# Optimization experiments

Measured on AMD Instinct MI355X. Metric: run time of the kernel, lower is better.

The kernel has to match this reference:

```python
import jax, jax.numpy as jnp
import numpy as np

B, I, H, T = 65536, 64, 64, 16  # batch, input_size, hidden_size, type_num


def setup_inputs() -> dict:
    key = jax.random.key(0)
    ks = jax.random.split(key, 10)
    s = 0.1  # ~1/sqrt(H) init scale like torch GRUCell
    return {
        "x": jax.random.normal(ks[0], (B, I), jnp.float32),
        "typ": jax.random.randint(ks[1], (B,), 0, T, jnp.int32),
        "c": jax.random.normal(ks[2], (B, H), jnp.float32),
        "registers": jax.random.normal(ks[3], (B, T, H), jnp.float32),
        # per-type GRUCell bank (stacked across types)
        "Wih": jax.random.normal(ks[4], (T, 3 * H, I), jnp.float32) * s,
        "Whh": jax.random.normal(ks[5], (T, 3 * H, H), jnp.float32) * s,
        "bih": jax.random.normal(ks[6], (T, 3 * H), jnp.float32) * s,
        "bhh": jax.random.normal(ks[7], (T, 3 * H), jnp.float32) * s,
        # core GRUCell: input = flattened registers (T*H)
        "cWih": jax.random.normal(ks[8], (3 * H, T * H), jnp.float32) * s,
        "cWhh": jax.random.normal(ks[9], (3 * H, H), jnp.float32) * s,
        "cbih": jnp.zeros((3 * H,), jnp.float32),
        "cbhh": jnp.zeros((3 * H,), jnp.float32),
    }


def _gru(gi, gh, h):
    # torch.nn.GRUCell math; gi/gh: (..., 3H), h: (..., H)
    ir, iz, in_ = jnp.split(gi, 3, axis=-1)
    hr, hz, hn = jnp.split(gh, 3, axis=-1)
    r = jax.nn.sigmoid(ir + hr)
    z = jax.nn.sigmoid(iz + hz)
    n = jnp.tanh(in_ + r * hn)
    return (1.0 - z) * n + z * h


def reference(x, typ, c, registers, Wih, Whh, bih, bhh, cWih, cWhh, cbih, cbhh):
    # Bank of T GRUCells, all run on the same input x with per-type hidden = registers[:, t]
    gi = jnp.einsum('bi,tgi->btg', x, Wih) + bih[None]            # (B,T,3H)
    gh = jnp.einsum('bth,tgh->btg', registers, Whh) + bhh[None]   # (B,T,3H)
    hidden_tmp = _gru(gi, gh, registers)                          # (B,T,H)

    # Gather/scatter register update: only slot typ[b] takes its GRU output,
    # all other slots keep the old register (exactly what hidden_all[N, I] does).
    mask = (jnp.arange(T)[None, :] == typ[:, None])[..., None]    # (B,T,1)
    reg_new = jnp.where(mask, hidden_tmp, registers)              # (B,T,H)

    # core_v2: core GRUCell over flattened registers with state c
    xflat = reg_new.reshape(B, T * H)
    cgi = xflat @ cWih.T + cbih
    cgh = c @ cWhh.T + cbhh
    core = _gru(cgi, cgh, c)                                      # (B,H)
    return core
```

## Files before the change

### kernel.cpp

```cpp
#include <hip/hip_runtime.h>
#include <hip/hip_bf16.h>

typedef unsigned short u16;
typedef unsigned int u32;
typedef __bf16 bf16x8 __attribute__((ext_vector_type(8)));
typedef float f32x4 __attribute__((ext_vector_type(4)));


__device__ __forceinline__ u16 f2bf(float f) {
  union { float f; u32 u; } v; v.f = f;
  u32 u = v.u;
  return (u16)((u + 0x7fffu + ((u >> 16) & 1u)) >> 16);
}
__device__ __forceinline__ float bf2f(u16 h) {
  union { u32 u; float f; } v; v.u = ((u32)h) << 16;
  return v.f;
}
__device__ __forceinline__ u32 pk2(float a, float b) {
  union { __hip_bfloat162 h; u32 u; } v;
  v.h = __float22bfloat162_rn(float2{a, b});
  return v.u;
}
__device__ __forceinline__ bf16x8 pack8(float4 a, float4 b) {
  union { u32 u[4]; bf16x8 v; } r;
  r.u[0] = pk2(a.x, a.y); r.u[1] = pk2(a.z, a.w);
  r.u[2] = pk2(b.x, b.y); r.u[3] = pk2(b.z, b.w);
  return r.v;
}
__device__ __forceinline__ float sigf(float x) { return 1.0f / (1.0f + __expf(-x)); }
__device__ __forceinline__ float tanh_fast(float x) { return 2.0f * sigf(2.0f * x) - 1.0f; }

__device__ __forceinline__ void gl_lds16(const void* g, void* l) {
  __builtin_amdgcn_global_load_lds(
      (const __attribute__((address_space(1))) unsigned int*)g,
      (__attribute__((address_space(3))) unsigned int*)l, 16, 0, 0);
}

__global__ __launch_bounds__(256) void k0_convert(
    const float* __restrict__ Wih, const float* __restrict__ Whh,
    const float* __restrict__ cWih, const float* __restrict__ cWhh,
    u16* __restrict__ wih_bf, u16* __restrict__ whh_bf,
    u16* __restrict__ cwih_bf, u16* __restrict__ cwhh_bf, int* __restrict__ gcnt)
{
  int i = blockIdx.x * 256 + threadIdx.x;
  if (blockIdx.x == 0 && threadIdx.x < 16) gcnt[threadIdx.x] = 0;
  if (i < 196608) {
    wih_bf[i]  = f2bf(Wih[i]);
    whh_bf[i]  = f2bf(Whh[i]);
    cwih_bf[i] = f2bf(cWih[i]);
  }
  if (i < 12288) cwhh_bf[i] = f2bf(cWhh[i]);
}

__global__ __launch_bounds__(256) void k_compact(
    const int* __restrict__ typ, int* __restrict__ gcnt, int* __restrict__ lists)
{
  __shared__ int cnt[16], base[16];
  const int tid = threadIdx.x;
  if (tid < 16) cnt[tid] = 0;
  __syncthreads();
  int r = blockIdx.x * 256 + tid;
  int t = typ[r];
  int rank = atomicAdd(&cnt[t], 1);
  __syncthreads();
  if (tid < 16) base[tid] = atomicAdd(&gcnt[tid], cnt[tid]);
  __syncthreads();
  lists[(size_t)t * 65536 + base[t] + rank] = r;
}

__global__ __launch_bounds__(256, 2) void k1_corr(
    const float* __restrict__ x, const float* __restrict__ regs,
    const u16* __restrict__ wih_bf, const u16* __restrict__ whh_bf,
    const float* __restrict__ bih, const float* __restrict__ bhh,
    const u16* __restrict__ cwih_bf,
    const int* __restrict__ gcnt, const int* __restrict__ lists,
    u16* __restrict__ corr)
{
  const int t = blockIdx.y;
  const int cnt = gcnt[t];
  const int ntiles = (cnt + 15) >> 4;

  const int tid = threadIdx.x;
  const int lane = tid & 63;
  const int w = tid >> 6;
  const int col = lane & 15;
  const int quad = lane >> 4;
  const int hidx = w * 16 + col;
  const f32x4 zero = {0.f, 0.f, 0.f, 0.f};

  bf16x8 bw[3][2], bh[3][2], bc[3][2];
  float vbi[3], vbh[3];
#pragma unroll
  for (int g = 0; g < 3; ++g) {
    const u16* pw = wih_bf + ((size_t)t * 192 + g * 64 + hidx) * 64;
    const u16* ph = whh_bf + ((size_t)t * 192 + g * 64 + hidx) * 64;
    const u16* pc = cwih_bf + (size_t)(g * 64 + hidx) * 1024 + t * 64;
#pragma unroll
    for (int ks = 0; ks < 2; ++ks) {
      bw[g][ks] = *(const bf16x8*)(pw + ks * 32 + quad * 8);
      bh[g][ks] = *(const bf16x8*)(ph + ks * 32 + quad * 8);
      bc[g][ks] = *(const bf16x8*)(pc + ks * 32 + quad * 8);
    }
    vbi[g] = bih[t * 192 + g * 64 + hidx];
    vbh[g] = bhh[t * 192 + g * 64 + hidx];
  }

  __shared__ int s_rows[16];
  __shared__ __align__(16) u16 sD[16 * 72];

  for (int tile = blockIdx.x; tile < ntiles; tile += 32) {
    __syncthreads();
    if (tid < 16) {
      int idx = tile * 16 + tid;
      s_rows[tid] = lists[(size_t)t * 65536 + (idx < cnt ? idx : cnt - 1)];
    }
    __syncthreads();

    const int ra = s_rows[col];
    f32x4 agi[3], agh[3];
#pragma unroll
    for (int g = 0; g < 3; ++g) { agi[g] = zero; agh[g] = zero; }
#pragma unroll
    for (int ks = 0; ks < 2; ++ks) {
      const float* xr = x + (size_t)ra * 64 + ks * 32 + quad * 8;
      const float* hr = regs + (size_t)ra * 1024 + t * 64 + ks * 32 + quad * 8;
      bf16x8 ax = pack8(*(const float4*)xr, *(const float4*)(xr + 4));
      bf16x8 ah = pack8(*(const float4*)hr, *(const float4*)(hr + 4));
#pragma unroll
      for (int g = 0; g < 3; ++g) {
        agi[g] = __builtin_amdgcn_mfma_f32_16x16x32_bf16(ax, bw[g][ks], agi[g], 0, 0, 0);
        agh[g] = __builtin_amdgcn_mfma_f32_16x16x32_bf16(ah, bh[g][ks], agh[g], 0, 0, 0);
      }
    }
#pragma unroll
    for (int rr = 0; rr < 4; ++rr) {
      int m = quad * 4 + rr;
      if (tile * 16 + m < cnt) {
        int r2 = s_rows[m];
        float ir  = agi[0][rr] + vbi[0];
        float iz  = agi[1][rr] + vbi[1];
        float in_ = agi[2][rr] + vbi[2];
        float hr  = agh[0][rr] + vbh[0];
        float hz  = agh[1][rr] + vbh[1];
        float hn  = agh[2][rr] + vbh[2];
        float rg = sigf(ir + hr);
        float zg = sigf(iz + hz);
        float ng = tanh_fast(in_ + rg * hn);
        float hold = regs[(size_t)r2 * 1024 + t * 64 + hidx];
        float hnew = (1.f - zg) * ng + zg * hold;
        sD[m * 72 + hidx] = f2bf(hnew - hold);
      }
    }
    __syncthreads();

    f32x4 acr[3];
#pragma unroll
    for (int g = 0; g < 3; ++g) acr[g] = zero;
#pragma unroll
    for (int ks = 0; ks < 2; ++ks) {
      bf16x8 ad = *(const bf16x8*)(&sD[col * 72 + ks * 32 + quad * 8]);
#pragma unroll
      for (int g = 0; g < 3; ++g)
        acr[g] = __builtin_amdgcn_mfma_f32_16x16x32_bf16(ad, bc[g][ks], acr[g], 0, 0, 0);
    }
#pragma unroll
    for (int rr = 0; rr < 4; ++rr) {
      int m = quad * 4 + rr;
      if (tile * 16 + m < cnt) {
        int r2 = s_rows[m];
#pragma unroll
        for (int g = 0; g < 3; ++g)
          corr[(size_t)r2 * 192 + g * 64 + hidx] = f2bf(acr[g][rr]);
      }
    }
  }
}

__global__ __launch_bounds__(256, 2) void k2_core(
    const float* __restrict__ regs, const float* __restrict__ c,
    const u16* __restrict__ cwih_bf, const u16* __restrict__ cwhh_bf,
    const float* __restrict__ cbih, const float* __restrict__ cbhh,
    const u16* __restrict__ corr, float* __restrict__ out)
{
  __shared__ __align__(16) float sA[2][4096];
  __shared__ __align__(16) u16  sB[2][12288];

  const int tid = threadIdx.x;
  const int b0 = blockIdx.x * 64;
  const int lane = tid & 63;
  const int wv = tid >> 6;
  const int col = lane & 15;
  const int quad = lane >> 4;
  const int hidx = wv * 16 + col;
  const f32x4 zero = {0.f, 0.f, 0.f, 0.f};

  {
#pragma unroll
    for (int s = 0; s < 4; ++s) {
      int i = s * 4 + wv;
      int r = i * 4 + (lane >> 4);
      int grp = lane & 15;
      gl_lds16(regs + (size_t)(b0 + r) * 1024 + ((grp ^ (r & 15)) << 2), &sA[0][i * 256]);
    }
#pragma unroll
    for (int s = 0; s < 6; ++s) {
      int j = s * 4 + wv;
      int n = j * 8 + (lane >> 3);
      int grp = lane & 7;
      gl_lds16(cwih_bf + (size_t)n * 1024 + ((grp ^ (n & 7)) << 3), &sB[0][j * 512]);
    }
  }

  f32x4 agh[4][3];
#pragma unroll
  for (int mt = 0; mt < 4; ++mt)
#pragma unroll
    for (int g = 0; g < 3; ++g) agh[mt][g] = zero;
#pragma unroll
  for (int ks = 0; ks < 2; ++ks) {
    bf16x8 bh2[3];
#pragma unroll
    for (int g = 0; g < 3; ++g)
      bh2[g] = *(const bf16x8*)(cwhh_bf + (size_t)(g * 64 + hidx) * 64 + ks * 32 + quad * 8);
#pragma unroll
    for (int mt = 0; mt < 4; ++mt) {
      const float* cr = c + (size_t)(b0 + mt * 16 + col) * 64 + ks * 32 + quad * 8;
      bf16x8 af = pack8(*(const float4*)cr, *(const float4*)(cr + 4));
#pragma unroll
      for (int g = 0; g < 3; ++g)
        agh[mt][g] = __builtin_amdgcn_mfma_f32_16x16x32_bf16(af, bh2[g], agh[mt][g], 0, 0, 0);
    }
  }

  f32x4 agi[4][3];
#pragma unroll
  for (int mt = 0; mt < 4; ++mt)
#pragma unroll
    for (int g = 0; g < 3; ++g) agi[mt][g] = zero;

  for (int kc = 0; kc < 16; ++kc) {
    __syncthreads();
    if (kc < 15) {
      float* sAn = sA[(kc + 1) & 1];
      u16*   sBn = sB[(kc + 1) & 1];
#pragma unroll
      for (int s = 0; s < 4; ++s) {
        int i = s * 4 + wv;
        int r = i * 4 + (lane >> 4);
        int grp = lane & 15;
        gl_lds16(regs + (size_t)(b0 + r) * 1024 + (kc + 1) * 64 + ((grp ^ (r & 15)) << 2),
                 sAn + i * 256);
      }
#pragma unroll
      for (int s = 0; s < 6; ++s) {
        int j = s * 4 + wv;
        int n = j * 8 + (lane >> 3);
        int grp = lane & 7;
        gl_lds16(cwih_bf + (size_t)n * 1024 + (kc + 1) * 64 + ((grp ^ (n & 7)) << 3),
                 sBn + j * 512);
      }
    }
    const float* sAc = sA[kc & 1];
    const u16*   sBc = sB[kc & 1];
#pragma unroll
    for (int ks = 0; ks < 2; ++ks) {
      bf16x8 bfr[3];
#pragma unroll
      for (int g = 0; g < 3; ++g) {
        int n = g * 64 + hidx;
        int grp = ks * 4 + quad;
        bfr[g] = *(const bf16x8*)(sBc + n * 64 + ((grp ^ (n & 7)) << 3));
      }
#pragma unroll
      for (int mt = 0; mt < 4; ++mt) {
        int r = mt * 16 + col;
        int g0 = ks * 8 + quad * 2;
        float4 q0 = *(const float4*)(sAc + r * 64 + (((g0    ) ^ (r & 15)) << 2));
        float4 q1 = *(const float4*)(sAc + r * 64 + (((g0 + 1) ^ (r & 15)) << 2));
        bf16x8 af = pack8(q0, q1);
#pragma unroll
        for (int g = 0; g < 3; ++g)
          agi[mt][g] = __builtin_amdgcn_mfma_f32_16x16x32_bf16(af, bfr[g], agi[mt][g], 0, 0, 0);
      }
    }
  }

  float e0 = cbih[hidx], e1 = cbih[64 + hidx], e2 = cbih[128 + hidx];
  float d0 = cbhh[hidx], d1 = cbhh[64 + hidx], d2 = cbhh[128 + hidx];
#pragma unroll
  for (int mt = 0; mt < 4; ++mt) {
#pragma unroll
    for (int rr = 0; rr < 4; ++rr) {
      int row = mt * 16 + quad * 4 + rr;
      size_t b = (size_t)(b0 + row);
      float ir  = agi[mt][0][rr] + e0 + bf2f(corr[b * 192 + hidx]);
      float iz  = agi[mt][1][rr] + e1 + bf2f(corr[b * 192 + 64 + hidx]);
      float in_ = agi[mt][2][rr] + e2 + bf2f(corr[b * 192 + 128 + hidx]);
      float hr  = agh[mt][0][rr] + d0;
      float hz  = agh[mt][1][rr] + d1;
      float hn  = agh[mt][2][rr] + d2;
      float rg = sigf(ir + hr);
      float zg = sigf(iz + hz);
      float ng = tanh_fast(in_ + rg * hn);
      float cold = c[b * 64 + hidx];
      out[b * 64 + hidx] = (1.f - zg) * ng + zg * cold;
    }
  }
}

extern "C" void kernel_launch(void* const* d_in, const int* in_sizes, int n_in,
                              void* d_out, int out_size, void* d_ws, size_t ws_size,
                              hipStream_t stream) {
  const float* x    = (const float*)d_in[0];
  const int*   typ  = (const int*)d_in[1];
  const float* c    = (const float*)d_in[2];
  const float* regs = (const float*)d_in[3];
  const float* Wih  = (const float*)d_in[4];
  const float* Whh  = (const float*)d_in[5];
  const float* bih  = (const float*)d_in[6];
  const float* bhh  = (const float*)d_in[7];
  const float* cWih = (const float*)d_in[8];
  const float* cWhh = (const float*)d_in[9];
  const float* cbih = (const float*)d_in[10];
  const float* cbhh = (const float*)d_in[11];
  float* out = (float*)d_out;

  char* ws = (char*)d_ws;
  u16* wih_bf  = (u16*)(ws + 0);
  u16* whh_bf  = (u16*)(ws + 393216);
  u16* cwih_bf = (u16*)(ws + 786432);
  u16* cwhh_bf = (u16*)(ws + 1179648);
  int* gcnt    = (int*)(ws + 1204224);
  int* lists   = (int*)(ws + 1204288);
  u16* corr    = (u16*)(ws + 5398592);

  k0_convert<<<768, 256, 0, stream>>>(Wih, Whh, cWih, cWhh,
                                      wih_bf, whh_bf, cwih_bf, cwhh_bf, gcnt);
  k_compact<<<256, 256, 0, stream>>>(typ, gcnt, lists);
  k1_corr<<<dim3(32, 16), 256, 0, stream>>>(x, regs, wih_bf, whh_bf, bih, bhh,
                                            cwih_bf, gcnt, lists, corr);
  k2_core<<<1024, 256, 0, stream>>>(regs, c, cwih_bf, cwhh_bf, cbih, cbhh, corr, out);
}
```

Baseline: 476.0 us.

## Fuse per-type GRU correction and core GRU into one type-grouped kernel

Merges the per-type correction kernel and the core GRU kernel into a single kernel that processes 64-row tiles of same-type rows. The per-type delta is kept in LDS and fed directly into the core input accumulator, so the bf16 corr buffer no longer round-trips through global memory and one launch disappears. Register rows are now gathered through the row list instead of read contiguously. The cWih tiles are read straight from global (L2) rather than staged in LDS. Each of the 72x16 blocks loops over several tiles with no cross-type load balancing, so uneven type counts can leave some blocks with more work.

```diff
diff --git a/kernel.cpp b/kernel.cpp
--- a/kernel.cpp
+++ b/kernel.cpp
@@ -11,10 +11,6 @@
   union { float f; u32 u; } v; v.f = f;
   u32 u = v.u;
   return (u16)((u + 0x7fffu + ((u >> 16) & 1u)) >> 16);
-}
-__device__ __forceinline__ float bf2f(u16 h) {
-  union { u32 u; float f; } v; v.u = ((u32)h) << 16;
-  return v.f;
 }
 __device__ __forceinline__ u32 pk2(float a, float b) {
   union { __hip_bfloat162 h; u32 u; } v;
@@ -68,125 +64,25 @@
   lists[(size_t)t * 65536 + base[t] + rank] = r;
 }
 
-__global__ __launch_bounds__(256, 2) void k1_corr(
+__global__ __launch_bounds__(256, 2) void k_fused(
     const float* __restrict__ x, const float* __restrict__ regs,
+    const float* __restrict__ c,
     const u16* __restrict__ wih_bf, const u16* __restrict__ whh_bf,
     const float* __restrict__ bih, const float* __restrict__ bhh,
-    const u16* __restrict__ cwih_bf,
+    const u16* __restrict__ cwih_bf, const u16* __restrict__ cwhh_bf,
+    const float* __restrict__ cbih, const float* __restrict__ cbhh,
     const int* __restrict__ gcnt, const int* __restrict__ lists,
-    u16* __restrict__ corr)
+    float* __restrict__ out)
 {
   const int t = blockIdx.y;
   const int cnt = gcnt[t];
-  const int ntiles = (cnt + 15) >> 4;
+  if ((int)blockIdx.x * 64 >= cnt) return;
+
+  __shared__ __align__(16) float sA[2][4096];
+  __shared__ __align__(16) u16  sD[4096];
+  __shared__ int s_rows[64];
 
   const int tid = threadIdx.x;
-  const int lane = tid & 63;
-  const int w = tid >> 6;
-  const int col = lane & 15;
-  const int quad = lane >> 4;
-  const int hidx = w * 16 + col;
-  const f32x4 zero = {0.f, 0.f, 0.f, 0.f};
-
-  bf16x8 bw[3][2], bh[3][2], bc[3][2];
-  float vbi[3], vbh[3];
-#pragma unroll
-  for (int g = 0; g < 3; ++g) {
-    const u16* pw = wih_bf + ((size_t)t * 192 + g * 64 + hidx) * 64;
-    const u16* ph = whh_bf + ((size_t)t * 192 + g * 64 + hidx) * 64;
-    const u16* pc = cwih_bf + (size_t)(g * 64 + hidx) * 1024 + t * 64;
-#pragma unroll
-    for (int ks = 0; ks < 2; ++ks) {
-      bw[g][ks] = *(const bf16x8*)(pw + ks * 32 + quad * 8);
-      bh[g][ks] = *(const bf16x8*)(ph + ks * 32 + quad * 8);
-      bc[g][ks] = *(const bf16x8*)(pc + ks * 32 + quad * 8);
-    }
-    vbi[g] = bih[t * 192 + g * 64 + hidx];
-    vbh[g] = bhh[t * 192 + g * 64 + hidx];
-  }
-
-  __shared__ int s_rows[16];
-  __shared__ __align__(16) u16 sD[16 * 72];
-
-  for (int tile = blockIdx.x; tile < ntiles; tile += 32) {
-    __syncthreads();
-    if (tid < 16) {
-      int idx = tile * 16 + tid;
-      s_rows[tid] = lists[(size_t)t * 65536 + (idx < cnt ? idx : cnt - 1)];
-    }
-    __syncthreads();
-
-    const int ra = s_rows[col];
-    f32x4 agi[3], agh[3];
-#pragma unroll
-    for (int g = 0; g < 3; ++g) { agi[g] = zero; agh[g] = zero; }
-#pragma unroll
-    for (int ks = 0; ks < 2; ++ks) {
-      const float* xr = x + (size_t)ra * 64 + ks * 32 + quad * 8;
-      const float* hr = regs + (size_t)ra * 1024 + t * 64 + ks * 32 + quad * 8;
-      bf16x8 ax = pack8(*(const float4*)xr, *(const float4*)(xr + 4));
-      bf16x8 ah = pack8(*(const float4*)hr, *(const float4*)(hr + 4));
-#pragma unroll
-      for (int g = 0; g < 3; ++g) {
-        agi[g] = __builtin_amdgcn_mfma_f32_16x16x32_bf16(ax, bw[g][ks], agi[g], 0, 0, 0);
-        agh[g] = __builtin_amdgcn_mfma_f32_16x16x32_bf16(ah, bh[g][ks], agh[g], 0, 0, 0);
-      }
-    }
-#pragma unroll
-    for (int rr = 0; rr < 4; ++rr) {
-      int m = quad * 4 + rr;
-      if (tile * 16 + m < cnt) {
-        int r2 = s_rows[m];
-        float ir  = agi[0][rr] + vbi[0];
-        float iz  = agi[1][rr] + vbi[1];
-        float in_ = agi[2][rr] + vbi[2];
-        float hr  = agh[0][rr] + vbh[0];
-        float hz  = agh[1][rr] + vbh[1];
-        float hn  = agh[2][rr] + vbh[2];
-        float rg = sigf(ir + hr);
-        float zg = sigf(iz + hz);
-        float ng = tanh_fast(in_ + rg * hn);
-        float hold = regs[(size_t)r2 * 1024 + t * 64 + hidx];
-        float hnew = (1.f - zg) * ng + zg * hold;
-        sD[m * 72 + hidx] = f2bf(hnew - hold);
-      }
-    }
-    __syncthreads();
-
-    f32x4 acr[3];
-#pragma unroll
-    for (int g = 0; g < 3; ++g) acr[g] = zero;
-#pragma unroll
-    for (int ks = 0; ks < 2; ++ks) {
-      bf16x8 ad = *(const bf16x8*)(&sD[col * 72 + ks * 32 + quad * 8]);
-#pragma unroll
-      for (int g = 0; g < 3; ++g)
-        acr[g] = __builtin_amdgcn_mfma_f32_16x16x32_bf16(ad, bc[g][ks], acr[g], 0, 0, 0);
-    }
-#pragma unroll
-    for (int rr = 0; rr < 4; ++rr) {
-      int m = quad * 4 + rr;
-      if (tile * 16 + m < cnt) {
-        int r2 = s_rows[m];
-#pragma unroll
-        for (int g = 0; g < 3; ++g)
-          corr[(size_t)r2 * 192 + g * 64 + hidx] = f2bf(acr[g][rr]);
-      }
-    }
-  }
-}
-
-__global__ __launch_bounds__(256, 2) void k2_core(
-    const float* __restrict__ regs, const float* __restrict__ c,
-    const u16* __restrict__ cwih_bf, const u16* __restrict__ cwhh_bf,
-    const float* __restrict__ cbih, const float* __restrict__ cbhh,
-    const u16* __restrict__ corr, float* __restrict__ out)
-{
-  __shared__ __align__(16) float sA[2][4096];
-  __shared__ __align__(16) u16  sB[2][12288];
-
-  const int tid = threadIdx.x;
-  const int b0 = blockIdx.x * 64;
   const int lane = tid & 63;
   const int wv = tid >> 6;
   const int col = lane & 15;
@@ -194,116 +90,170 @@
   const int hidx = wv * 16 + col;
   const f32x4 zero = {0.f, 0.f, 0.f, 0.f};
 
-  {
-#pragma unroll
-    for (int s = 0; s < 4; ++s) {
-      int i = s * 4 + wv;
-      int r = i * 4 + (lane >> 4);
-      int grp = lane & 15;
-      gl_lds16(regs + (size_t)(b0 + r) * 1024 + ((grp ^ (r & 15)) << 2), &sA[0][i * 256]);
-    }
-#pragma unroll
-    for (int s = 0; s < 6; ++s) {
-      int j = s * 4 + wv;
-      int n = j * 8 + (lane >> 3);
-      int grp = lane & 7;
-      gl_lds16(cwih_bf + (size_t)n * 1024 + ((grp ^ (n & 7)) << 3), &sB[0][j * 512]);
-    }
+  bf16x8 bw[3][2], bh[3][2], bc[3][2];
+  float vbi[3], vbh[3];
+#pragma unroll
+  for (int g = 0; g < 3; ++g) {
+    const u16* pw = wih_bf + ((size_t)t * 192 + g * 64 + hidx) * 64;
+    const u16* ph = whh_bf + ((size_t)t * 192 + g * 64 + hidx) * 64;
+    const u16* pc = cwih_bf + (size_t)(g * 64 + hidx) * 1024 + t * 64;
+#pragma unroll
+    for (int ks = 0; ks < 2; ++ks) {
+      bw[g][ks] = *(const bf16x8*)(pw + ks * 32 + quad * 8);
+      bh[g][ks] = *(const bf16x8*)(ph + ks * 32 + quad * 8);
+      bc[g][ks] = *(const bf16x8*)(pc + ks * 32 + quad * 8);
+    }
+    vbi[g] = bih[t * 192 + g * 64 + hidx];
+    vbh[g] = bhh[t * 192 + g * 64 + hidx];
   }
-
-  f32x4 agh[4][3];
-#pragma unroll
-  for (int mt = 0; mt < 4; ++mt)
-#pragma unroll
-    for (int g = 0; g < 3; ++g) agh[mt][g] = zero;
-#pragma unroll
-  for (int ks = 0; ks < 2; ++ks) {
-    bf16x8 bh2[3];
-#pragma unroll
-    for (int g = 0; g < 3; ++g)
-      bh2[g] = *(const bf16x8*)(cwhh_bf + (size_t)(g * 64 + hidx) * 64 + ks * 32 + quad * 8);
-#pragma unroll
+  const float e0 = cbih[hidx], e1 = cbih[64 + hidx], e2 = cbih[128 + hidx];
+  const float d0 = cbhh[hidx], d1 = cbhh[64 + hidx], d2 = cbhh[128 + hidx];
+
+  for (int tile = blockIdx.x; tile * 64 < cnt; tile += (int)gridDim.x) {
+    __syncthreads();
+    if (tid < 64) {
+      int idx = tile * 64 + tid;
+      s_rows[tid] = lists[(size_t)t * 65536 + (idx < cnt ? idx : cnt - 1)];
+    }
+    __syncthreads();
+
+    const int grp = lane & 15;
+    const int rsw = wv * 4 + quad;
+    const float* pA[4];
+#pragma unroll
+    for (int s = 0; s < 4; ++s)
+      pA[s] = regs + (size_t)s_rows[s * 16 + wv * 4 + quad] * 1024 + ((grp ^ rsw) << 2);
+
+#pragma unroll
+    for (int s = 0; s < 4; ++s)
+      gl_lds16(pA[s], &sA[0][(s * 4 + wv) * 256]);
+
+#pragma unroll 2
     for (int mt = 0; mt < 4; ++mt) {
-      const float* cr = c + (size_t)(b0 + mt * 16 + col) * 64 + ks * 32 + quad * 8;
-      bf16x8 af = pack8(*(const float4*)cr, *(const float4*)(cr + 4));
+      const int ra = s_rows[mt * 16 + col];
+      f32x4 agi1[3], agh1[3];
+#pragma unroll
+      for (int g = 0; g < 3; ++g) { agi1[g] = zero; agh1[g] = zero; }
+#pragma unroll
+      for (int ks = 0; ks < 2; ++ks) {
+        const float* xr = x + (size_t)ra * 64 + ks * 32 + quad * 8;
+        const float* hr = regs + (size_t)ra * 1024 + t * 64 + ks * 32 + quad * 8;
+        bf16x8 ax = pack8(*(const float4*)xr, *(const float4*)(xr + 4));
+        bf16x8 ah = pack8(*(const float4*)hr, *(const float4*)(hr + 4));
+#pragma unroll
+        for (int g = 0; g < 3; ++g) {
+          agi1[g] = __builtin_amdgcn_mfma_f32_16x16x32_bf16(ax, bw[g][ks], agi1[g], 0, 0, 0);
+          agh1[g] = __builtin_amdgcn_mfma_f32_16x16x32_bf16(ah, bh[g][ks], agh1[g], 0, 0, 0);
+        }
+      }
+#pragma unroll
+      for (int rr = 0; rr < 4; ++rr) {
+        const int m = mt * 16 + quad * 4 + rr;
+        const int r2 = s_rows[m];
+        float ir  = agi1[0][rr] + vbi[0];
+        float iz  = agi1[1][rr] + vbi[1];
+        float in_ = agi1[2][rr] + vbi[2];
+        float hr2 = agh1[0][rr] + vbh[0];
+        float hz  = agh1[1][rr] + vbh[1];
+        float hn  = agh1[2][rr] + vbh[2];
+        float rg = sigf(ir + hr2);
+        float zg = sigf(iz + hz);
+        float ng = tanh_fast(in_ + rg * hn);
+        float hold = regs[(size_t)r2 * 1024 + t * 64 + hidx];
+        float hnew = (1.f - zg) * ng + zg * hold;
+        sD[m * 64 + (((hidx >> 3) ^ (m & 7)) << 3) + (hidx & 7)] = f2bf(hnew - hold);
+      }
+    }
+
+    f32x4 agh[4][3];
+#pragma unroll
+    for (int mt = 0; mt < 4; ++mt)
+#pragma unroll
+      for (int g = 0; g < 3; ++g) agh[mt][g] = zero;
+#pragma unroll
+    for (int ks = 0; ks < 2; ++ks) {
+      bf16x8 bh2[3];
 #pragma unroll
       for (int g = 0; g < 3; ++g)
-        agh[mt][g] = __builtin_amdgcn_mfma_f32_16x16x32_bf16(af, bh2[g], agh[mt][g], 0, 0, 0);
-    }
-  }
-
-  f32x4 agi[4][3];
-#pragma unroll
-  for (int mt = 0; mt < 4; ++mt)
-#pragma unroll
-    for (int g = 0; g < 3; ++g) agi[mt][g] = zero;
-
-  for (int kc = 0; kc < 16; ++kc) {
+        bh2[g] = *(const bf16x8*)(cwhh_bf + (size_t)(g * 64 + hidx) * 64 + ks * 32 + quad * 8);
+#pragma unroll
+      for (int mt = 0; mt < 4; ++mt) {
+        const float* cr = c + (size_t)s_rows[mt * 16 + col] * 64 + ks * 32 + quad * 8;
+        bf16x8 af = pack8(*(const float4*)cr, *(const float4*)(cr + 4));
+#pragma unroll
+        for (int g = 0; g < 3; ++g)
+          agh[mt][g] = __builtin_amdgcn_mfma_f32_16x16x32_bf16(af, bh2[g], agh[mt][g], 0, 0, 0);
+      }
+    }
+
     __syncthreads();
-    if (kc < 15) {
-      float* sAn = sA[(kc + 1) & 1];
-      u16*   sBn = sB[(kc + 1) & 1];
-#pragma unroll
-      for (int s = 0; s < 4; ++s) {
-        int i = s * 4 + wv;
-        int r = i * 4 + (lane >> 4);
-        int grp = lane & 15;
-        gl_lds16(regs + (size_t)(b0 + r) * 1024 + (kc + 1) * 64 + ((grp ^ (r & 15)) << 2),
-                 sAn + i * 256);
-      }
-#pragma unroll
-      for (int s = 0; s < 6; ++s) {
-        int j = s * 4 + wv;
-        int n = j * 8 + (lane >> 3);
-        int grp = lane & 7;
-        gl_lds16(cwih_bf + (size_t)n * 1024 + (kc + 1) * 64 + ((grp ^ (n & 7)) << 3),
-                 sBn + j * 512);
-      }
-    }
-    const float* sAc = sA[kc & 1];
-    const u16*   sBc = sB[kc & 1];
+
+    f32x4 agi[4][3];
+#pragma unroll
+    for (int mt = 0; mt < 4; ++mt)
+#pragma unroll
+      for (int g = 0; g < 3; ++g) agi[mt][g] = zero;
 #pragma unroll
     for (int ks = 0; ks < 2; ++ks) {
-      bf16x8 bfr[3];
-#pragma unroll
-      for (int g = 0; g < 3; ++g) {
-        int n = g * 64 + hidx;
-        int grp = ks * 4 + quad;
-        bfr[g] = *(const bf16x8*)(sBc + n * 64 + ((grp ^ (n & 7)) << 3));
-      }
 #pragma unroll
       for (int mt = 0; mt < 4; ++mt) {
-        int r = mt * 16 + col;
-        int g0 = ks * 8 + quad * 2;
-        float4 q0 = *(const float4*)(sAc + r * 64 + (((g0    ) ^ (r & 15)) << 2));
-        float4 q1 = *(const float4*)(sAc + r * 64 + (((g0 + 1) ^ (r & 15)) << 2));
-        bf16x8 af = pack8(q0, q1);
+        const int m = mt * 16 + col;
+        bf16x8 ad = *(const bf16x8*)(&sD[m * 64 + (((ks * 4 + quad) ^ (m & 7)) << 3)]);
 #pragma unroll
         for (int g = 0; g < 3; ++g)
-          agi[mt][g] = __builtin_amdgcn_mfma_f32_16x16x32_bf16(af, bfr[g], agi[mt][g], 0, 0, 0);
-      }
-    }
-  }
-
-  float e0 = cbih[hidx], e1 = cbih[64 + hidx], e2 = cbih[128 + hidx];
-  float d0 = cbhh[hidx], d1 = cbhh[64 + hidx], d2 = cbhh[128 + hidx];
-#pragma unroll
-  for (int mt = 0; mt < 4; ++mt) {
-#pragma unroll
-    for (int rr = 0; rr < 4; ++rr) {
-      int row = mt * 16 + quad * 4 + rr;
-      size_t b = (size_t)(b0 + row);
-      float ir  = agi[mt][0][rr] + e0 + bf2f(corr[b * 192 + hidx]);
-      float iz  = agi[mt][1][rr] + e1 + bf2f(corr[b * 192 + 64 + hidx]);
-      float in_ = agi[mt][2][rr] + e2 + bf2f(corr[b * 192 + 128 + hidx]);
-      float hr  = agh[mt][0][rr] + d0;
-      float hz  = agh[mt][1][rr] + d1;
-      float hn  = agh[mt][2][rr] + d2;
-      float rg = sigf(ir + hr);
-      float zg = sigf(iz + hz);
-      float ng = tanh_fast(in_ + rg * hn);
-      float cold = c[b * 64 + hidx];
-      out[b * 64 + hidx] = (1.f - zg) * ng + zg * cold;
+          agi[mt][g] = __builtin_amdgcn_mfma_f32_16x16x32_bf16(ad, bc[g][ks], agi[mt][g], 0, 0, 0);
+      }
+    }
+
+    for (int kc = 0; kc < 16; ++kc) {
+      __syncthreads();
+      if (kc < 15) {
+        float* sAn = sA[(kc + 1) & 1];
+#pragma unroll
+        for (int s = 0; s < 4; ++s)
+          gl_lds16(pA[s] + (kc + 1) * 64, sAn + (s * 4 + wv) * 256);
+      }
+      const float* sAc = sA[kc & 1];
+#pragma unroll
+      for (int ks = 0; ks < 2; ++ks) {
+        bf16x8 bfr[3];
+#pragma unroll
+        for (int g = 0; g < 3; ++g)
+          bfr[g] = *(const bf16x8*)(cwih_bf + (size_t)(g * 64 + hidx) * 1024 + kc * 64 + ks * 32 + quad * 8);
+#pragma unroll
+        for (int mt = 0; mt < 4; ++mt) {
+          const int r = mt * 16 + col;
+          const int g0 = ks * 8 + quad * 2;
+          float4 q0 = *(const float4*)(sAc + r * 64 + (((g0    ) ^ (r & 15)) << 2));
+          float4 q1 = *(const float4*)(sAc + r * 64 + (((g0 + 1) ^ (r & 15)) << 2));
+          bf16x8 af = pack8(q0, q1);
+#pragma unroll
+          for (int g = 0; g < 3; ++g)
+            agi[mt][g] = __builtin_amdgcn_mfma_f32_16x16x32_bf16(af, bfr[g], agi[mt][g], 0, 0, 0);
+        }
+      }
+    }
+
+#pragma unroll
+    for (int mt = 0; mt < 4; ++mt) {
+#pragma unroll
+      for (int rr = 0; rr < 4; ++rr) {
+        const int m = mt * 16 + quad * 4 + rr;
+        if (tile * 64 + m < cnt) {
+          const size_t b = (size_t)s_rows[m];
+          float ir  = agi[mt][0][rr] + e0;
+          float iz  = agi[mt][1][rr] + e1;
+          float in_ = agi[mt][2][rr] + e2;
+          float hr2 = agh[mt][0][rr] + d0;
+          float hz  = agh[mt][1][rr] + d1;
+          float hn  = agh[mt][2][rr] + d2;
+          float rg = sigf(ir + hr2);
+          float zg = sigf(iz + hz);
+          float ng = tanh_fast(in_ + rg * hn);
+          float cold = c[b * 64 + hidx];
+          out[b * 64 + hidx] = (1.f - zg) * ng + zg * cold;
+        }
+      }
     }
   }
 }
@@ -332,12 +282,10 @@
   u16* cwhh_bf = (u16*)(ws + 1179648);
   int* gcnt    = (int*)(ws + 1204224);
   int* lists   = (int*)(ws + 1204288);
-  u16* corr    = (u16*)(ws + 5398592);
 
   k0_convert<<<768, 256, 0, stream>>>(Wih, Whh, cWih, cWhh,
                                       wih_bf, whh_bf, cwih_bf, cwhh_bf, gcnt);
   k_compact<<<256, 256, 0, stream>>>(typ, gcnt, lists);
-  k1_corr<<<dim3(32, 16), 256, 0, stream>>>(x, regs, wih_bf, whh_bf, bih, bhh,
-                                            cwih_bf, gcnt, lists, corr);
-  k2_core<<<1024, 256, 0, stream>>>(regs, c, cwih_bf, cwhh_bf, cbih, cbhh, corr, out);
-}
+  k_fused<<<dim3(72, 16), 256, 0, stream>>>(x, regs, c, wih_bf, whh_bf, bih, bhh,
+                                            cwih_bf, cwhh_bf, cbih, cbhh, gcnt, lists, out);
+}
```

Result: slower. 564.3 us (+18.6%).

## Substitute updated register slot directly in core GEMM load instead of correction term

Applied to the files above, without the earlier changes.

Instead of computing a per-row correction (hnew-hold) projected through cWih in k1 and adding it in k2, k1 now writes the fp32 new hidden state for the selected slot, and k2 picks, per row and K-chunk, whether to load from registers or from that slot buffer. This removes the correction MFMA, its LDS staging and sync, and the bf16 corr write and read. It also avoids bf16 rounding of the difference term. In exchange, k2 takes per-lane address selection and reads typ.

```diff
diff --git a/kernel.cpp b/kernel.cpp
--- a/kernel.cpp
+++ b/kernel.cpp
@@ -11,10 +11,6 @@
   union { float f; u32 u; } v; v.f = f;
   u32 u = v.u;
   return (u16)((u + 0x7fffu + ((u >> 16) & 1u)) >> 16);
-}
-__device__ __forceinline__ float bf2f(u16 h) {
-  union { u32 u; float f; } v; v.u = ((u32)h) << 16;
-  return v.f;
 }
 __device__ __forceinline__ u32 pk2(float a, float b) {
   union { __hip_bfloat162 h; u32 u; } v;
@@ -68,13 +64,12 @@
   lists[(size_t)t * 65536 + base[t] + rank] = r;
 }
 
-__global__ __launch_bounds__(256, 2) void k1_corr(
+__global__ __launch_bounds__(256, 2) void k1_gru(
     const float* __restrict__ x, const float* __restrict__ regs,
     const u16* __restrict__ wih_bf, const u16* __restrict__ whh_bf,
     const float* __restrict__ bih, const float* __restrict__ bhh,
-    const u16* __restrict__ cwih_bf,
     const int* __restrict__ gcnt, const int* __restrict__ lists,
-    u16* __restrict__ corr)
+    float* __restrict__ modslot)
 {
   const int t = blockIdx.y;
   const int cnt = gcnt[t];
@@ -88,25 +83,22 @@
   const int hidx = w * 16 + col;
   const f32x4 zero = {0.f, 0.f, 0.f, 0.f};
 
-  bf16x8 bw[3][2], bh[3][2], bc[3][2];
+  bf16x8 bw[3][2], bh[3][2];
   float vbi[3], vbh[3];
 #pragma unroll
   for (int g = 0; g < 3; ++g) {
     const u16* pw = wih_bf + ((size_t)t * 192 + g * 64 + hidx) * 64;
     const u16* ph = whh_bf + ((size_t)t * 192 + g * 64 + hidx) * 64;
-    const u16* pc = cwih_bf + (size_t)(g * 64 + hidx) * 1024 + t * 64;
 #pragma unroll
     for (int ks = 0; ks < 2; ++ks) {
       bw[g][ks] = *(const bf16x8*)(pw + ks * 32 + quad * 8);
       bh[g][ks] = *(const bf16x8*)(ph + ks * 32 + quad * 8);
-      bc[g][ks] = *(const bf16x8*)(pc + ks * 32 + quad * 8);
     }
     vbi[g] = bih[t * 192 + g * 64 + hidx];
     vbh[g] = bhh[t * 192 + g * 64 + hidx];
   }
 
   __shared__ int s_rows[16];
-  __shared__ __align__(16) u16 sD[16 * 72];
 
   for (int tile = blockIdx.x; tile < ntiles; tile += 32) {
     __syncthreads();
@@ -148,29 +140,7 @@
         float ng = tanh_fast(in_ + rg * hn);
         float hold = regs[(size_t)r2 * 1024 + t * 64 + hidx];
         float hnew = (1.f - zg) * ng + zg * hold;
-        sD[m * 72 + hidx] = f2bf(hnew - hold);
-      }
-    }
-    __syncthreads();
-
-    f32x4 acr[3];
-#pragma unroll
-    for (int g = 0; g < 3; ++g) acr[g] = zero;
-#pragma unroll
-    for (int ks = 0; ks < 2; ++ks) {
-      bf16x8 ad = *(const bf16x8*)(&sD[col * 72 + ks * 32 + quad * 8]);
-#pragma unroll
-      for (int g = 0; g < 3; ++g)
-        acr[g] = __builtin_amdgcn_mfma_f32_16x16x32_bf16(ad, bc[g][ks], acr[g], 0, 0, 0);
-    }
-#pragma unroll
-    for (int rr = 0; rr < 4; ++rr) {
-      int m = quad * 4 + rr;
-      if (tile * 16 + m < cnt) {
-        int r2 = s_rows[m];
-#pragma unroll
-        for (int g = 0; g < 3; ++g)
-          corr[(size_t)r2 * 192 + g * 64 + hidx] = f2bf(acr[g][rr]);
+        modslot[(size_t)r2 * 64 + hidx] = hnew;
       }
     }
   }
@@ -178,9 +148,10 @@
 
 __global__ __launch_bounds__(256, 2) void k2_core(
     const float* __restrict__ regs, const float* __restrict__ c,
+    const int* __restrict__ typ, const float* __restrict__ modslot,
     const u16* __restrict__ cwih_bf, const u16* __restrict__ cwhh_bf,
     const float* __restrict__ cbih, const float* __restrict__ cbhh,
-    const u16* __restrict__ corr, float* __restrict__ out)
+    float* __restrict__ out)
 {
   __shared__ __align__(16) float sA[2][4096];
   __shared__ __align__(16) u16  sB[2][12288];
@@ -194,20 +165,32 @@
   const int hidx = wv * 16 + col;
   const f32x4 zero = {0.f, 0.f, 0.f, 0.f};
 
+  const int grp = lane & 15;
+  const float* pA[4];
+  const float* pM[4];
+  int t4[4];
+#pragma unroll
+  for (int s = 0; s < 4; ++s) {
+    int i = s * 4 + wv;
+    int r = i * 4 + (lane >> 4);
+    int swz = (grp ^ (r & 15)) << 2;
+    pA[s] = regs + (size_t)(b0 + r) * 1024 + swz;
+    pM[s] = modslot + (size_t)(b0 + r) * 64 + swz;
+    t4[s] = typ[b0 + r];
+  }
+
   {
 #pragma unroll
     for (int s = 0; s < 4; ++s) {
-      int i = s * 4 + wv;
-      int r = i * 4 + (lane >> 4);
-      int grp = lane & 15;
-      gl_lds16(regs + (size_t)(b0 + r) * 1024 + ((grp ^ (r & 15)) << 2), &sA[0][i * 256]);
+      const float* src = (t4[s] == 0) ? pM[s] : pA[s];
+      gl_lds16(src, &sA[0][(s * 4 + wv) * 256]);
     }
 #pragma unroll
     for (int s = 0; s < 6; ++s) {
       int j = s * 4 + wv;
       int n = j * 8 + (lane >> 3);
-      int grp = lane & 7;
-      gl_lds16(cwih_bf + (size_t)n * 1024 + ((grp ^ (n & 7)) << 3), &sB[0][j * 512]);
+      int grpb = lane & 7;
+      gl_lds16(cwih_bf + (size_t)n * 1024 + ((grpb ^ (n & 7)) << 3), &sB[0][j * 512]);
     }
   }
 
@@ -245,18 +228,15 @@
       u16*   sBn = sB[(kc + 1) & 1];
 #pragma unroll
       for (int s = 0; s < 4; ++s) {
-        int i = s * 4 + wv;
-        int r = i * 4 + (lane >> 4);
-        int grp = lane & 15;
-        gl_lds16(regs + (size_t)(b0 + r) * 1024 + (kc + 1) * 64 + ((grp ^ (r & 15)) << 2),
-                 sAn + i * 256);
+        const float* src = (t4[s] == kc + 1) ? pM[s] : (pA[s] + (kc + 1) * 64);
+        gl_lds16(src, sAn + (s * 4 + wv) * 256);
       }
 #pragma unroll
       for (int s = 0; s < 6; ++s) {
         int j = s * 4 + wv;
         int n = j * 8 + (lane >> 3);
-        int grp = lane & 7;
-        gl_lds16(cwih_bf + (size_t)n * 1024 + (kc + 1) * 64 + ((grp ^ (n & 7)) << 3),
+        int grpb = lane & 7;
+        gl_lds16(cwih_bf + (size_t)n * 1024 + (kc + 1) * 64 + ((grpb ^ (n & 7)) << 3),
                  sBn + j * 512);
       }
     }
@@ -268,8 +248,8 @@
 #pragma unroll
       for (int g = 0; g < 3; ++g) {
         int n = g * 64 + hidx;
-        int grp = ks * 4 + quad;
-        bfr[g] = *(const bf16x8*)(sBc + n * 64 + ((grp ^ (n & 7)) << 3));
+        int grpb = ks * 4 + quad;
+        bfr[g] = *(const bf16x8*)(sBc + n * 64 + ((grpb ^ (n & 7)) << 3));
       }
 #pragma unroll
       for (int mt = 0; mt < 4; ++mt) {
@@ -293,9 +273,9 @@
     for (int rr = 0; rr < 4; ++rr) {
       int row = mt * 16 + quad * 4 + rr;
       size_t b = (size_t)(b0 + row);
-      float ir  = agi[mt][0][rr] + e0 + bf2f(corr[b * 192 + hidx]);
-      float iz  = agi[mt][1][rr] + e1 + bf2f(corr[b * 192 + 64 + hidx]);
-      float in_ = agi[mt][2][rr] + e2 + bf2f(corr[b * 192 + 128 + hidx]);
+      float ir  = agi[mt][0][rr] + e0;
+      float iz  = agi[mt][1][rr] + e1;
+      float in_ = agi[mt][2][rr] + e2;
       float hr  = agh[mt][0][rr] + d0;
       float hz  = agh[mt][1][rr] + d1;
       float hn  = agh[mt][2][rr] + d2;
@@ -332,12 +312,13 @@
   u16* cwhh_bf = (u16*)(ws + 1179648);
   int* gcnt    = (int*)(ws + 1204224);
   int* lists   = (int*)(ws + 1204288);
-  u16* corr    = (u16*)(ws + 5398592);
+  float* modslot = (float*)(ws + 5398592);
 
   k0_convert<<<768, 256, 0, stream>>>(Wih, Whh, cWih, cWhh,
                                       wih_bf, whh_bf, cwih_bf, cwhh_bf, gcnt);
   k_compact<<<256, 256, 0, stream>>>(typ, gcnt, lists);
-  k1_corr<<<dim3(32, 16), 256, 0, stream>>>(x, regs, wih_bf, whh_bf, bih, bhh,
-                                            cwih_bf, gcnt, lists, corr);
-  k2_core<<<1024, 256, 0, stream>>>(regs, c, cwih_bf, cwhh_bf, cbih, cbhh, corr, out);
-}
+  k1_gru<<<dim3(32, 16), 256, 0, stream>>>(x, regs, wih_bf, whh_bf, bih, bhh,
+                                           gcnt, lists, modslot);
+  k2_core<<<1024, 256, 0, stream>>>(regs, c, typ, modslot, cwih_bf, cwhh_bf,
+                                    cbih, cbhh, out);
+}
```

Result: no change. 467.8 us (-1.7%).
